# Performance work log

Hardware: AMD Instinct MI355X
Metric: run time of the kernel (lower is better)

## Reference

```python
import jax, jax.numpy as jnp
import numpy as np

EPS = 1e-12  # F.normalize clamp_min eps

def _l2norm(v, axis):
    return v / jnp.maximum(jnp.linalg.norm(v, axis=axis, keepdims=True), EPS)

def setup_inputs() -> dict:
    key = jax.random.key(0)
    k1, k2, k3, k4 = jax.random.split(key, 4)
    N, C, H, W, K = 256, 128, 31, 31, 64
    x = jax.random.normal(k1, (N, C, H, W), dtype=jnp.float32)
    conv_w = jax.random.normal(k2, (K, C), dtype=jnp.float32) * 0.1   # 1x1 conv weight, no bias (vladv2=False)
    centroids = jax.random.uniform(k3, (K, C), dtype=jnp.float32)     # torch.rand init
    atten_w = jax.random.normal(k4, (C,), dtype=jnp.float32) * 0.1    # attention 1x1 conv weight
    atten_b = jnp.zeros((1,), dtype=jnp.float32)
    return {"x": x, "conv_w": conv_w, "centroids": centroids, "atten_w": atten_w, "atten_b": atten_b}

def reference(x, conv_w, centroids, atten_w, atten_b):
    N, C, H, W = x.shape
    S = H * W  # 961
    # attention head: ReLU -> Conv2d(C,1,1) -> ReLU
    hmp = jax.nn.relu(jnp.einsum('nchw,c->nhw', jax.nn.relu(x), atten_w) + atten_b[0])
    hmp_f = hmp.reshape(N, S)                     # [N,S]
    # normalize input over channel dim
    xn = _l2norm(x, axis=1)
    x_f = xn.reshape(N, C, S)                     # [N,C,S]
    x_mul = x_f * hmp_f[:, None, :]               # [N,C,S] (hmp applied once)
    # soft assignment: 1x1 conv (no bias) on xn*hmp, softmax over clusters
    soft_assign = jax.nn.softmax(jnp.einsum('kc,ncs->nks', conv_w, x_mul), axis=1)
    # fused weighted residual aggregation (hmp applied a second time, as in source)
    w = soft_assign * hmp_f[:, None, :]           # [N,K,S]
    vlad = jnp.einsum('nks,ncs->nkc', w, x_mul) - centroids[None, :, :] * jnp.sum(w, axis=-1)[:, :, None]
    vlad = _l2norm(vlad, axis=2)                  # intra-normalize per cluster
    vlad = vlad.reshape(N, -1)
    vlad = _l2norm(vlad, axis=1)
    vlad = _l2norm(vlad, axis=1)                  # source normalizes flattened vlad twice
    return vlad
```

## Files before the change

### kernel.cpp

```cpp
#include <hip/hip_runtime.h>
#include <hip/hip_bf16.h>

#define N_ 256
#define C_ 128
#define S_ 961
#define K_ 64
#define TS 64
#define NTILE_LOC 8
#define NTHREADS 512

typedef __attribute__((ext_vector_type(4))) float f32x4;
typedef __attribute__((ext_vector_type(8))) _Float16 f16x8;
typedef __attribute__((ext_vector_type(4))) _Float16 f16x4;

#define MFMAF(a, b, c) __builtin_amdgcn_mfma_f32_16x16x32_f16((a), (b), (c), 0, 0, 0)

template <bool ATOMIC>
__global__ __launch_bounds__(NTHREADS, 8) void vlad_main(
    const float* __restrict__ x,
    const float* __restrict__ conv_w,
    const float* __restrict__ cent,
    const float* __restrict__ aw,
    const float* __restrict__ ab,
    float* __restrict__ out,
    float* __restrict__ ws)
{
    __shared__ _Float16 s_xs[C_][72];
    __shared__ __align__(16) unsigned char s_xtu[TS * 136 * sizeof(_Float16)];
    _Float16 (*s_xT)[136] = (_Float16 (*)[136])s_xtu;
    _Float16 (*s_u)[72]   = (_Float16 (*)[72])s_xtu;
    __shared__ _Float16 s_cw[16][64][8];
    __shared__ float s_ared[2][8][68];
    __shared__ float s_cs[8][68];
    __shared__ float s_wp[8][4][8];
    __shared__ float s_wsum[K_];

    const int tid = threadIdx.x;
    const int bid = blockIdx.x;
    const int n = bid >> 1, h = bid & 1;
    const int sbase = h * (NTILE_LOC * TS);
    const int lane = tid & 63;
    const int w = tid >> 6;
    const int la = lane & 15;
    const int lg = lane >> 4;
    const float bias = ab[0];
    const float* xn = x + (size_t)n * (C_ * S_);

    const int cb = tid >> 4;
    const int c0 = cb * 4;
    const int s0l = (tid & 15) * 4;

    float awr[4];
    #pragma unroll
    for (int r = 0; r < 4; ++r) awr[r] = aw[c0 + r];

    {
        int b = tid >> 5;
        int mt = b >> 2, cc = b & 3;
        #pragma unroll
        for (int dl = 0; dl < 2; ++dl) {
            int l = (tid & 31) * 2 + dl;
            const float* p = conv_w + ((l & 15) + 16 * mt) * C_ + 8 * (l >> 4) + 32 * cc;
            f16x8 v;
            #pragma unroll
            for (int i = 0; i < 8; ++i) v[i] = (_Float16)p[i];
            *(f16x8*)&s_cw[b][l][0] = v;
        }
    }

    const int nt1 = w & 3;
    const int mtb = (w >> 2) * 2;
    const int sc = 16 * nt1 + la;

    const int mtb2 = (w & 1) * 2;
    const int ctb2 = (w >> 1) * 2;
    f32x4 acc2[2][2];
    #pragma unroll
    for (int m = 0; m < 2; ++m)
        #pragma unroll
        for (int ci = 0; ci < 2; ++ci) acc2[m][ci] = (f32x4){0.f, 0.f, 0.f, 0.f};

    float wp0[4] = {0.f, 0.f, 0.f, 0.f};
    float wp1[4] = {0.f, 0.f, 0.f, 0.f};

    for (int T = 0; T < NTILE_LOC; ++T) {
        {
            int gs = sbase + T * TS + s0l;
            f16x4 hv[4];
            float ssqp[4] = {0.f, 0.f, 0.f, 0.f};
            float hdp[4]  = {0.f, 0.f, 0.f, 0.f};
            #pragma unroll
            for (int r = 0; r < 4; ++r) {
                const float* pr = xn + (size_t)(c0 + r) * S_ + gs;
                float f0, f1, f2, f3;
                if (gs + 3 < S_) {
                    f0 = pr[0]; f1 = pr[1]; f2 = pr[2]; f3 = pr[3];
                } else {
                    f0 = (gs + 0 < S_) ? pr[0] : 0.f;
                    f1 = (gs + 1 < S_) ? pr[1] : 0.f;
                    f2 = (gs + 2 < S_) ? pr[2] : 0.f;
                    f3 = (gs + 3 < S_) ? pr[3] : 0.f;
                }
                f16x4 v = {(_Float16)f0, (_Float16)f1, (_Float16)f2, (_Float16)f3};
                hv[r] = v;
                ssqp[0] += f0 * f0; ssqp[1] += f1 * f1;
                ssqp[2] += f2 * f2; ssqp[3] += f3 * f3;
                hdp[0] += fmaxf(f0, 0.f) * awr[r];
                hdp[1] += fmaxf(f1, 0.f) * awr[r];
                hdp[2] += fmaxf(f2, 0.f) * awr[r];
                hdp[3] += fmaxf(f3, 0.f) * awr[r];
                *(f16x4*)&s_xs[c0 + r][s0l] = v;
            }
            #pragma unroll
            for (int j = 0; j < 4; ++j) {
                int srow = s0l + j;
                int cidx = c0 ^ (((srow >> 3) & 3) << 3);
                f16x4 vT = {hv[0][j], hv[1][j], hv[2][j], hv[3][j]};
                *(f16x4*)&s_xT[srow][cidx] = vT;
            }
            #pragma unroll
            for (int j = 0; j < 4; ++j) {
                ssqp[j] += __shfl_xor(ssqp[j], 16);
                ssqp[j] += __shfl_xor(ssqp[j], 32);
                hdp[j]  += __shfl_xor(hdp[j], 16);
                hdp[j]  += __shfl_xor(hdp[j], 32);
            }
            if (lg == 0) {
                f32x4 a = {ssqp[0], ssqp[1], ssqp[2], ssqp[3]};
                f32x4 b = {hdp[0], hdp[1], hdp[2], hdp[3]};
                *(f32x4*)&s_ared[0][w][s0l] = a;
                *(f32x4*)&s_ared[1][w][s0l] = b;
            }
        }
        __syncthreads();

        float e0[4], e1[4], hm, al, csw;
        {
            int swz = ((sc >> 3) & 3) << 3;
            f32x4 d0 = {0.f, 0.f, 0.f, 0.f}, d1 = {0.f, 0.f, 0.f, 0.f};
            #pragma unroll
            for (int cc = 0; cc < 4; ++cc) {
                f16x8 a0 = *(const f16x8*)&s_cw[(mtb + 0) * 4 + cc][lane][0];
                f16x8 a1 = *(const f16x8*)&s_cw[(mtb + 1) * 4 + cc][lane][0];
                f16x8 b  = *(const f16x8*)&s_xT[sc][(8 * lg + 32 * cc) ^ swz];
                d0 = MFMAF(a0, b, d0);
                d1 = MFMAF(a1, b, d1);
            }
            float ssq = s_ared[0][2 * lg][sc] + s_ared[0][2 * lg + 1][sc];
            float hd  = s_ared[1][2 * lg][sc] + s_ared[1][2 * lg + 1][sc];
            ssq += __shfl_xor(ssq, 16); ssq += __shfl_xor(ssq, 32);
            hd  += __shfl_xor(hd, 16);  hd  += __shfl_xor(hd, 32);
            int sg = sbase + T * TS + sc;
            hm = (sg < S_) ? fmaxf(hd + bias, 0.f) : 0.f;
            al = hm / fmaxf(sqrtf(ssq), 1e-12f);
            float cs = 0.f;
            #pragma unroll
            for (int i = 0; i < 4; ++i) {
                e0[i] = __expf(d0[i] * al);
                e1[i] = __expf(d1[i] * al);
                cs += e0[i] + e1[i];
            }
            cs += __shfl_xor(cs, 16); cs += __shfl_xor(cs, 32);
            csw = cs;
            if (lg == 0) s_cs[w][sc] = cs;
        }
        __syncthreads();

        {
            float cst = csw + s_cs[w ^ 4][sc];
            float wl = hm * __builtin_amdgcn_rcpf(cst);
            #pragma unroll
            for (int i = 0; i < 4; ++i) {
                float wv0 = e0[i] * wl;
                float wv1 = e1[i] * wl;
                wp0[i] += wv0;
                wp1[i] += wv1;
                s_u[16 * mtb + 4 * lg + i][sc]       = (_Float16)(wv0 * al);
                s_u[16 * (mtb + 1) + 4 * lg + i][sc] = (_Float16)(wv1 * al);
            }
        }
        __syncthreads();

        {
            #pragma unroll
            for (int sc2 = 0; sc2 < 2; ++sc2) {
                f16x8 ua[2];
                #pragma unroll
                for (int m = 0; m < 2; ++m)
                    ua[m] = *(const f16x8*)&s_u[la + 16 * (mtb2 + m)][8 * lg + 32 * sc2];
                #pragma unroll
                for (int ci = 0; ci < 2; ++ci) {
                    f16x8 xb = *(const f16x8*)&s_xs[la + 16 * (ctb2 + ci)][8 * lg + 32 * sc2];
                    #pragma unroll
                    for (int m = 0; m < 2; ++m)
                        acc2[m][ci] = MFMAF(ua[m], xb, acc2[m][ci]);
                }
            }
        }
        __syncthreads();
    }

    {
        #pragma unroll
        for (int i = 0; i < 4; ++i) {
            #pragma unroll
            for (int m = 1; m < 16; m <<= 1) {
                wp0[i] += __shfl_xor(wp0[i], m);
                wp1[i] += __shfl_xor(wp1[i], m);
            }
        }
        if (la == 0) {
            #pragma unroll
            for (int i = 0; i < 4; ++i) {
                s_wp[w][lg][i]     = wp0[i];
                s_wp[w][lg][4 + i] = wp1[i];
            }
        }
    }
    __syncthreads();
    if (tid < K_) {
        int k = tid;
        int kh = k >> 5, m2 = (k >> 4) & 1, lgk = (k >> 2) & 3, ik = k & 3;
        float v = 0.f;
        #pragma unroll
        for (int q = 0; q < 4; ++q) v += s_wp[4 * kh + q][lgk][4 * m2 + ik];
        s_wsum[k] = v;
    }
    __syncthreads();

    {
        float* dst = ATOMIC ? out : (h ? ws : out);
        #pragma unroll
        for (int m = 0; m < 2; ++m) {
            #pragma unroll
            for (int ci = 0; ci < 2; ++ci) {
                int c = la + 16 * (ctb2 + ci);
                #pragma unroll
                for (int i = 0; i < 4; ++i) {
                    int k = 16 * (mtb2 + m) + 4 * lg + i;
                    float val = acc2[m][ci][i] - cent[k * C_ + c] * s_wsum[k];
                    size_t off = (size_t)n * (K_ * C_) + k * C_ + c;
                    if (ATOMIC) atomicAdd(&dst[off], val);
                    else dst[off] = val;
                }
            }
        }
    }
}

template <bool WS>
__global__ __launch_bounds__(256) void vlad_norm(
    float* __restrict__ out, const float* __restrict__ ws)
{
    __shared__ float s_rs[K_], s_f[K_];
    __shared__ float s_fin;
    const int n = blockIdx.x, tid = threadIdx.x;
    const int k = tid >> 2, q = tid & 3;
    float* po = out + (size_t)n * (K_ * C_) + k * C_ + q * 32;
    const float* pw = ws + (size_t)n * (K_ * C_) + k * C_ + q * 32;

    float v[32];
    float ssq = 0.f;
    #pragma unroll
    for (int i = 0; i < 8; ++i) {
        f32x4 a = *(const f32x4*)&po[4 * i];
        if (WS) {
            f32x4 b = *(const f32x4*)&pw[4 * i];
            a[0]+=b[0]; a[1]+=b[1]; a[2]+=b[2]; a[3]+=b[3];
        }
        #pragma unroll
        for (int j = 0; j < 4; ++j) { v[4*i+j] = a[j]; ssq += a[j]*a[j]; }
    }
    ssq += __shfl_xor(ssq, 1);
    ssq += __shfl_xor(ssq, 2);
    if (q == 0) {
        float rs = 1.0f / fmaxf(sqrtf(ssq), 1e-12f);
        s_rs[k] = rs;
        s_f[k] = ssq * rs * rs;
    }
    __syncthreads();
    if (tid < 64) {
        float f = s_f[tid];
        #pragma unroll
        for (int m = 1; m < 64; m <<= 1) f += __shfl_xor(f, m);
        if (tid == 0) {
            float n1 = sqrtf(f);
            float sc1 = 1.0f / fmaxf(n1, 1e-12f);
            float n2 = n1 * sc1;
            float sc2 = 1.0f / fmaxf(n2, 1e-12f);
            s_fin = sc1 * sc2;
        }
    }
    __syncthreads();
    float sc = s_rs[k] * s_fin;
    #pragma unroll
    for (int i = 0; i < 8; ++i) {
        f32x4 a = {v[4*i]*sc, v[4*i+1]*sc, v[4*i+2]*sc, v[4*i+3]*sc};
        *(f32x4*)&po[4 * i] = a;
    }
}

extern "C" void kernel_launch(void* const* d_in, const int* in_sizes, int n_in,
                              void* d_out, int out_size, void* d_ws, size_t ws_size,
                              hipStream_t stream) {
    const float* x      = (const float*)d_in[0];
    const float* conv_w = (const float*)d_in[1];
    const float* cent   = (const float*)d_in[2];
    const float* aw     = (const float*)d_in[3];
    const float* ab     = (const float*)d_in[4];
    float* outp = (float*)d_out;
    float* wsp  = (float*)d_ws;

    const size_t need = (size_t)N_ * K_ * C_ * sizeof(float);
    if (ws_size >= need) {
        vlad_main<false><<<2 * N_, NTHREADS, 0, stream>>>(x, conv_w, cent, aw, ab, outp, wsp);
        vlad_norm<true><<<N_, 256, 0, stream>>>(outp, wsp);
    } else {
        hipMemsetAsync(d_out, 0, need, stream);
        vlad_main<true><<<2 * N_, NTHREADS, 0, stream>>>(x, conv_w, cent, aw, ab, outp, wsp);
        vlad_norm<false><<<N_, 256, 0, stream>>>(outp, nullptr);
    }
}
```

Baseline: 55.74 us.

## Swizzle LDS tiles without padding and reduce partial sums via shared atomics

Removes the row padding from the x tile and its transposed copy and applies XOR swizzles keyed on the row's low bits, so bank conflicts are avoided without extra LDS. The per-warp partial sum-of-squares and attention dot products are now accumulated with LDS atomics into one 64-entry buffer instead of a per-warp array followed by cross-lane shuffles. It also shrinks the column-sum scratch. Less LDS per block may allow more resident blocks, but the LDS atomics and the extra zeroing and barrier add serialization.

```diff
diff --git a/kernel.cpp b/kernel.cpp
--- a/kernel.cpp
+++ b/kernel.cpp
@@ -15,7 +15,7 @@
 
 #define MFMAF(a, b, c) __builtin_amdgcn_mfma_f32_16x16x32_f16((a), (b), (c), 0, 0, 0)
 
-template <bool ATOMIC>
+template <int MODE>
 __global__ __launch_bounds__(NTHREADS, 8) void vlad_main(
     const float* __restrict__ x,
     const float* __restrict__ conv_w,
@@ -25,13 +25,13 @@
     float* __restrict__ out,
     float* __restrict__ ws)
 {
-    __shared__ _Float16 s_xs[C_][72];
-    __shared__ __align__(16) unsigned char s_xtu[TS * 136 * sizeof(_Float16)];
-    _Float16 (*s_xT)[136] = (_Float16 (*)[136])s_xtu;
+    __shared__ _Float16 s_xs[C_][64];
+    __shared__ __align__(16) unsigned char s_xtu[TS * 128 * sizeof(_Float16)];
+    _Float16 (*s_xT)[128] = (_Float16 (*)[128])s_xtu;
     _Float16 (*s_u)[72]   = (_Float16 (*)[72])s_xtu;
     __shared__ _Float16 s_cw[16][64][8];
-    __shared__ float s_ared[2][8][68];
-    __shared__ float s_cs[8][68];
+    __shared__ float s_ared2[2][64];
+    __shared__ float s_cs[8][18];
     __shared__ float s_wp[8][4][8];
     __shared__ float s_wsum[K_];
 
@@ -67,6 +67,8 @@
             *(f16x8*)&s_cw[b][l][0] = v;
         }
     }
+    if (tid < 128) ((float*)s_ared2)[tid] = 0.f;
+    __syncthreads();
 
     const int nt1 = w & 3;
     const int mtb = (w >> 2) * 2;
@@ -109,12 +111,13 @@
                 hdp[1] += fmaxf(f1, 0.f) * awr[r];
                 hdp[2] += fmaxf(f2, 0.f) * awr[r];
                 hdp[3] += fmaxf(f3, 0.f) * awr[r];
-                *(f16x4*)&s_xs[c0 + r][s0l] = v;
+                int c = c0 + r;
+                *(f16x4*)&s_xs[c][s0l ^ ((c & 7) << 3)] = v;
             }
             #pragma unroll
             for (int j = 0; j < 4; ++j) {
                 int srow = s0l + j;
-                int cidx = c0 ^ (((srow >> 3) & 3) << 3);
+                int cidx = c0 ^ ((srow & 7) << 3);
                 f16x4 vT = {hv[0][j], hv[1][j], hv[2][j], hv[3][j]};
                 *(f16x4*)&s_xT[srow][cidx] = vT;
             }
@@ -126,17 +129,18 @@
                 hdp[j]  += __shfl_xor(hdp[j], 32);
             }
             if (lg == 0) {
-                f32x4 a = {ssqp[0], ssqp[1], ssqp[2], ssqp[3]};
-                f32x4 b = {hdp[0], hdp[1], hdp[2], hdp[3]};
-                *(f32x4*)&s_ared[0][w][s0l] = a;
-                *(f32x4*)&s_ared[1][w][s0l] = b;
+                #pragma unroll
+                for (int j = 0; j < 4; ++j) {
+                    atomicAdd(&s_ared2[0][s0l + j], ssqp[j]);
+                    atomicAdd(&s_ared2[1][s0l + j], hdp[j]);
+                }
             }
         }
         __syncthreads();
 
         float e0[4], e1[4], hm, al, csw;
         {
-            int swz = ((sc >> 3) & 3) << 3;
+            int swz = (sc & 7) << 3;
             f32x4 d0 = {0.f, 0.f, 0.f, 0.f}, d1 = {0.f, 0.f, 0.f, 0.f};
             #pragma unroll
             for (int cc = 0; cc < 4; ++cc) {
@@ -146,10 +150,8 @@
                 d0 = MFMAF(a0, b, d0);
                 d1 = MFMAF(a1, b, d1);
             }
-            float ssq = s_ared[0][2 * lg][sc] + s_ared[0][2 * lg + 1][sc];
-            float hd  = s_ared[1][2 * lg][sc] + s_ared[1][2 * lg + 1][sc];
-            ssq += __shfl_xor(ssq, 16); ssq += __shfl_xor(ssq, 32);
-            hd  += __shfl_xor(hd, 16);  hd  += __shfl_xor(hd, 32);
+            float ssq = s_ared2[0][sc];
+            float hd  = s_ared2[1][sc];
             int sg = sbase + T * TS + sc;
             hm = (sg < S_) ? fmaxf(hd + bias, 0.f) : 0.f;
             al = hm / fmaxf(sqrtf(ssq), 1e-12f);
@@ -162,12 +164,13 @@
             }
             cs += __shfl_xor(cs, 16); cs += __shfl_xor(cs, 32);
             csw = cs;
-            if (lg == 0) s_cs[w][sc] = cs;
+            if (lg == 0) s_cs[w][la] = cs;
         }
         __syncthreads();
 
         {
-            float cst = csw + s_cs[w ^ 4][sc];
+            if (tid < 128) ((float*)s_ared2)[tid] = 0.f;
+            float cst = csw + s_cs[w ^ 4][la];
             float wl = hm * __builtin_amdgcn_rcpf(cst);
             #pragma unroll
             for (int i = 0; i < 4; ++i) {
@@ -190,7 +193,8 @@
                     ua[m] = *(const f16x8*)&s_u[la + 16 * (mtb2 + m)][8 * lg + 32 * sc2];
                 #pragma unroll
                 for (int ci = 0; ci < 2; ++ci) {
-                    f16x8 xb = *(const f16x8*)&s_xs[la + 16 * (ctb2 + ci)][8 * lg + 32 * sc2];
+                    int c = la + 16 * (ctb2 + ci);
+                    f16x8 xb = *(const f16x8*)&s_xs[c][(8 * lg + 32 * sc2) ^ ((c & 7) << 3)];
                     #pragma unroll
                     for (int m = 0; m < 2; ++m)
                         acc2[m][ci] = MFMAF(ua[m], xb, acc2[m][ci]);
@@ -229,9 +233,8 @@
     __syncthreads();
 
     {
-        float* dst = ATOMIC ? out : (h ? ws : out);
-        #pragma unroll
-        for (int m = 0; m < 2; ++m) {
+        #pragma unroll
+        for (int m = 0; m < 2; ++m)
             #pragma unroll
             for (int ci = 0; ci < 2; ++ci) {
                 int c = la + 16 * (ctb2 + ci);
@@ -240,11 +243,10 @@
                     int k = 16 * (mtb2 + m) + 4 * lg + i;
                     float val = acc2[m][ci][i] - cent[k * C_ + c] * s_wsum[k];
                     size_t off = (size_t)n * (K_ * C_) + k * C_ + c;
-                    if (ATOMIC) atomicAdd(&dst[off], val);
-                    else dst[off] = val;
+                    if (MODE == 2) atomicAdd(&out[off], val);
+                    else { float* dst = (h ? ws : out); dst[off] = val; }
                 }
             }
-        }
     }
 }
 
@@ -311,13 +313,14 @@
     float* outp = (float*)d_out;
     float* wsp  = (float*)d_ws;
 
-    const size_t need = (size_t)N_ * K_ * C_ * sizeof(float);
-    if (ws_size >= need) {
-        vlad_main<false><<<2 * N_, NTHREADS, 0, stream>>>(x, conv_w, cent, aw, ab, outp, wsp);
+    const size_t part = (size_t)N_ * K_ * C_ * sizeof(float);
+
+    if (ws_size >= part) {
+        vlad_main<0><<<2 * N_, NTHREADS, 0, stream>>>(x, conv_w, cent, aw, ab, outp, wsp);
         vlad_norm<true><<<N_, 256, 0, stream>>>(outp, wsp);
     } else {
-        hipMemsetAsync(d_out, 0, need, stream);
-        vlad_main<true><<<2 * N_, NTHREADS, 0, stream>>>(x, conv_w, cent, aw, ab, outp, wsp);
+        hipMemsetAsync(d_out, 0, part, stream);
+        vlad_main<2><<<2 * N_, NTHREADS, 0, stream>>>(x, conv_w, cent, aw, ab, outp, wsp);
         vlad_norm<false><<<N_, 256, 0, stream>>>(outp, nullptr);
     }
 }
```

Result: slower. 76.91 us (+38.0%).
